# Performance work log

Measured on AMD Instinct MI355X. Metric: run time of the kernel, lower is better.

## Reference

```python
import jax, jax.numpy as jnp
import numpy as np

N, M, D = 8192, 8192, 256

def setup_inputs() -> dict:
    key = jax.random.key(0)
    kx, ky = jax.random.split(key)
    x = jax.random.normal(kx, (N, D), dtype=jnp.float32)
    y = jax.random.normal(ky, (M, D), dtype=jnp.float32)
    gamma = jnp.float32(1.0)  # learnable scalar parameter
    return {"x": x, "y": y, "gamma": gamma}

def reference(x, y, gamma):
    # Flatten trailing dims (matches x.view(x.size(0), -1))
    x = x.reshape(x.shape[0], -1)
    y = y.reshape(y.shape[0], -1)
    x_sq = jnp.sum(x * x, axis=-1)  # [N]
    y_sq = jnp.sum(y * y, axis=-1)  # [M]
    xy = x @ y.T                    # [N, M]
    sqdist = jnp.maximum(x_sq[:, None] + y_sq[None, :] - 2.0 * xy, 0.0)
    return jnp.exp(-gamma * sqdist)
```

## Files before the change

### kernel.cpp

```cpp
#include <hip/hip_runtime.h>
#include <stdint.h>


typedef __attribute__((ext_vector_type(4))) float f32x4;
typedef __attribute__((ext_vector_type(8))) int   i32x8;

#define NN 8192
#define MM 8192
#define DD 256
#define BK 128

__global__ __launch_bounds__(256) void prep_kernel(
    const float* __restrict__ x, const float* __restrict__ y,
    unsigned char* __restrict__ xb, unsigned char* __restrict__ yb,
    float* __restrict__ xsq, float* __restrict__ ysq) {
  const int lane = threadIdx.x & 63;
  const int row  = blockIdx.x * 4 + (threadIdx.x >> 6);

  const float* src = x;
  unsigned char* dst = xb;
  float* sq = xsq;
  int r = row;
  if (row >= NN) { src = y; dst = yb; sq = ysq; r = row - NN; }

  const float4 v = reinterpret_cast<const float4*>(src + (size_t)r * DD)[lane];
  float s = v.x * v.x + v.y * v.y + v.z * v.z + v.w * v.w;

  int w = 0;
  w = __builtin_amdgcn_cvt_pk_fp8_f32(v.x, v.y, w, false);
  w = __builtin_amdgcn_cvt_pk_fp8_f32(v.z, v.w, w, true);
  reinterpret_cast<int*>(dst + (size_t)r * DD)[lane] = w;

  #pragma unroll
  for (int o = 32; o > 0; o >>= 1) s += __shfl_down(s, o);
  if (lane == 0) sq[r] = s;
}

__global__ __launch_bounds__(256, 2) void rbf_gemm_kernel(
    const unsigned char* __restrict__ xb, const unsigned char* __restrict__ yb,
    const float* __restrict__ xsq, const float* __restrict__ ysq,
    const float* __restrict__ gamma, float* __restrict__ out) {
  __shared__ unsigned char As[128 * BK];
  __shared__ unsigned char Bs[128 * BK];

  const int tid   = threadIdx.x;
  const int lane  = tid & 63;
  const int wave  = tid >> 6;
  const int waveM = wave >> 1;
  const int waveN = wave & 1;
  const int row0  = blockIdx.y * 128;
  const int col0  = blockIdx.x * 128;

  f32x4 acc[4][4] = {};

  const int srow = lane >> 3;
  const int spos = lane & 7;
  const int sseg = ((spos & 1) | (((spos >> 1) ^ (srow & 3)) << 1)) * 16;

  const int fm = lane & 15;
  const int g  = lane >> 4;
  const int foff = fm * 128 + ((g ^ (fm & 3)) * 32);

  #pragma unroll
  for (int kt = 0; kt < 2; ++kt) {
    const int kk = kt * BK;
    __syncthreads();
    #pragma unroll
    for (int q = 0; q < 2; ++q) {
      const int c = wave * 2 + q;
      #pragma unroll
      for (int p = 0; p < 2; ++p) {
        const unsigned char* ga =
            yb + (size_t)(col0 + c * 16 + p * 8 + srow) * DD + kk + sseg;
        __builtin_amdgcn_global_load_lds(
            (const __attribute__((address_space(1))) void*)ga,
            (__attribute__((address_space(3))) void*)(As + c * 2048 + p * 1024),
            16, 0, 0);
        const unsigned char* gb =
            xb + (size_t)(row0 + c * 16 + p * 8 + srow) * DD + kk + sseg;
        __builtin_amdgcn_global_load_lds(
            (const __attribute__((address_space(1))) void*)gb,
            (__attribute__((address_space(3))) void*)(Bs + c * 2048 + p * 1024),
            16, 0, 0);
      }
    }
    __syncthreads();

    i32x8 a[4], b[4];
    #pragma unroll
    for (int i = 0; i < 4; ++i)
      a[i] = *reinterpret_cast<const i32x8*>(As + (waveM * 4 + i) * 2048 + foff);
    #pragma unroll
    for (int j = 0; j < 4; ++j)
      b[j] = *reinterpret_cast<const i32x8*>(Bs + (waveN * 4 + j) * 2048 + foff);

    #pragma unroll
    for (int i = 0; i < 4; ++i)
      #pragma unroll
      for (int j = 0; j < 4; ++j)
        acc[i][j] = __builtin_amdgcn_mfma_scale_f32_16x16x128_f8f6f4(
            a[i], b[j], acc[i][j], 0, 0,
            0, 0x7F7F7F7F, 0, 0x7F7F7F7F);
  }

  const float gm = gamma[0];
  const int rowb = row0 + waveN * 64 + (lane & 15);
  const int colq = col0 + waveM * 64 + (lane >> 4) * 4;

  float xsv[4];
  #pragma unroll
  for (int j = 0; j < 4; ++j) xsv[j] = xsq[rowb + j * 16];
  float4 ysv[4];
  #pragma unroll
  for (int i = 0; i < 4; ++i)
    ysv[i] = *reinterpret_cast<const float4*>(ysq + colq + i * 16);

  #pragma unroll
  for (int j = 0; j < 4; ++j) {
    const size_t obase = (size_t)(rowb + j * 16) * MM;
    #pragma unroll
    for (int i = 0; i < 4; ++i) {
      float4 v;
      float s;
      s = xsv[j] + ysv[i].x - 2.0f * acc[i][j][0]; v.x = __expf(-gm * fmaxf(s, 0.0f));
      s = xsv[j] + ysv[i].y - 2.0f * acc[i][j][1]; v.y = __expf(-gm * fmaxf(s, 0.0f));
      s = xsv[j] + ysv[i].z - 2.0f * acc[i][j][2]; v.z = __expf(-gm * fmaxf(s, 0.0f));
      s = xsv[j] + ysv[i].w - 2.0f * acc[i][j][3]; v.w = __expf(-gm * fmaxf(s, 0.0f));
      *reinterpret_cast<float4*>(out + obase + colq + i * 16) = v;
    }
  }
}

extern "C" void kernel_launch(void* const* d_in, const int* in_sizes, int n_in,
                              void* d_out, int out_size, void* d_ws, size_t ws_size,
                              hipStream_t stream) {
  const float* x     = (const float*)d_in[0];
  const float* y     = (const float*)d_in[1];
  const float* gamma = (const float*)d_in[2];
  float* out = (float*)d_out;

  unsigned char* xb = (unsigned char*)d_ws;
  unsigned char* yb = xb + (size_t)NN * DD;
  float* xsq = (float*)(yb + (size_t)MM * DD);
  float* ysq = xsq + NN;

  prep_kernel<<<(NN + MM) / 4, 256, 0, stream>>>(x, y, xb, yb, xsq, ysq);

  dim3 grid(MM / 128, NN / 128);
  rbf_gemm_kernel<<<grid, 256, 0, stream>>>(xb, yb, xsq, ysq, gamma, out);
}
```

Before: 284.0 us.

## Load FP8 MFMA fragments directly from global memory, dropping LDS staging

Removes the shared-memory tiles and the global_load_lds staging with its barriers. Each wave now reads its i32x8 MFMA fragments straight from global memory (L2/L1 cached), and occupancy is raised to 3 blocks per CU. The kernel is dominated by writing the 256 MB fp32 output, so this mainly cuts sync and LDS overhead. The cost is redundant global reads of the operand tiles across the two waves that share them.

```diff
diff --git a/kernel.cpp b/kernel.cpp
--- a/kernel.cpp
+++ b/kernel.cpp
@@ -8,7 +8,6 @@
 #define NN 8192
 #define MM 8192
 #define DD 256
-#define BK 128
 
 __global__ __launch_bounds__(256) void prep_kernel(
     const float* __restrict__ x, const float* __restrict__ y,
@@ -36,13 +35,10 @@
   if (lane == 0) sq[r] = s;
 }
 
-__global__ __launch_bounds__(256, 2) void rbf_gemm_kernel(
+__global__ __launch_bounds__(256, 3) void rbf_gemm_kernel(
     const unsigned char* __restrict__ xb, const unsigned char* __restrict__ yb,
     const float* __restrict__ xsq, const float* __restrict__ ysq,
     const float* __restrict__ gamma, float* __restrict__ out) {
-  __shared__ unsigned char As[128 * BK];
-  __shared__ unsigned char Bs[128 * BK];
-
   const int tid   = threadIdx.x;
   const int lane  = tid & 63;
   const int wave  = tid >> 6;
@@ -51,48 +47,26 @@
   const int row0  = blockIdx.y * 128;
   const int col0  = blockIdx.x * 128;
 
-  f32x4 acc[4][4] = {};
-
-  const int srow = lane >> 3;
-  const int spos = lane & 7;
-  const int sseg = ((spos & 1) | (((spos >> 1) ^ (srow & 3)) << 1)) * 16;
-
   const int fm = lane & 15;
   const int g  = lane >> 4;
-  const int foff = fm * 128 + ((g ^ (fm & 3)) * 32);
+
+  const unsigned char* abase =
+      yb + (size_t)(col0 + waveM * 64 + fm) * DD + g * 32;
+  const unsigned char* bbase =
+      xb + (size_t)(row0 + waveN * 64 + fm) * DD + g * 32;
+
+  f32x4 acc[4][4] = {};
 
   #pragma unroll
   for (int kt = 0; kt < 2; ++kt) {
-    const int kk = kt * BK;
-    __syncthreads();
-    #pragma unroll
-    for (int q = 0; q < 2; ++q) {
-      const int c = wave * 2 + q;
-      #pragma unroll
-      for (int p = 0; p < 2; ++p) {
-        const unsigned char* ga =
-            yb + (size_t)(col0 + c * 16 + p * 8 + srow) * DD + kk + sseg;
-        __builtin_amdgcn_global_load_lds(
-            (const __attribute__((address_space(1))) void*)ga,
-            (__attribute__((address_space(3))) void*)(As + c * 2048 + p * 1024),
-            16, 0, 0);
-        const unsigned char* gb =
-            xb + (size_t)(row0 + c * 16 + p * 8 + srow) * DD + kk + sseg;
-        __builtin_amdgcn_global_load_lds(
-            (const __attribute__((address_space(1))) void*)gb,
-            (__attribute__((address_space(3))) void*)(Bs + c * 2048 + p * 1024),
-            16, 0, 0);
-      }
-    }
-    __syncthreads();
-
+    const int kk = kt * 128;
     i32x8 a[4], b[4];
     #pragma unroll
     for (int i = 0; i < 4; ++i)
-      a[i] = *reinterpret_cast<const i32x8*>(As + (waveM * 4 + i) * 2048 + foff);
+      a[i] = *reinterpret_cast<const i32x8*>(abase + (size_t)i * 16 * DD + kk);
     #pragma unroll
     for (int j = 0; j < 4; ++j)
-      b[j] = *reinterpret_cast<const i32x8*>(Bs + (waveN * 4 + j) * 2048 + foff);
+      b[j] = *reinterpret_cast<const i32x8*>(bbase + (size_t)j * 16 * DD + kk);
 
     #pragma unroll
     for (int i = 0; i < 4; ++i)
```

Result: slower. 323.3 us (+13.8%).

## Process two column tiles per block with double-buffered LDS and overlapped epilogue

Applied to the files above, without the earlier changes.

Each block now computes a 128x256 output region as two 128-column tiles. The x-tile is staged once for both K halves and reused across both column tiles. The y-tile loads are double-buffered so the next global-to-LDS load is issued before the current MFMA compute, and the first tile's exp epilogue and stores run while the second tile's loads are in flight. This halves x reloads and hides load latency behind compute and stores, at the cost of twice the LDS (64KB), a second accumulator set raising register pressure, and half as many blocks.

```diff
diff --git a/kernel.cpp b/kernel.cpp
--- a/kernel.cpp
+++ b/kernel.cpp
@@ -40,8 +40,8 @@
     const unsigned char* __restrict__ xb, const unsigned char* __restrict__ yb,
     const float* __restrict__ xsq, const float* __restrict__ ysq,
     const float* __restrict__ gamma, float* __restrict__ out) {
-  __shared__ unsigned char As[128 * BK];
-  __shared__ unsigned char Bs[128 * BK];
+  __shared__ unsigned char Bs[2 * 128 * BK];
+  __shared__ unsigned char As[2][128 * BK];
 
   const int tid   = threadIdx.x;
   const int lane  = tid & 63;
@@ -49,9 +49,7 @@
   const int waveM = wave >> 1;
   const int waveN = wave & 1;
   const int row0  = blockIdx.y * 128;
-  const int col0  = blockIdx.x * 128;
-
-  f32x4 acc[4][4] = {};
+  const int col0  = blockIdx.x * 256;
 
   const int srow = lane >> 3;
   const int spos = lane & 7;
@@ -61,39 +59,45 @@
   const int g  = lane >> 4;
   const int foff = fm * 128 + ((g ^ (fm & 3)) * 32);
 
-  #pragma unroll
-  for (int kt = 0; kt < 2; ++kt) {
-    const int kk = kt * BK;
-    __syncthreads();
+  auto stageA = [&](unsigned char* dstbuf, int colt, int kk) {
     #pragma unroll
     for (int q = 0; q < 2; ++q) {
       const int c = wave * 2 + q;
       #pragma unroll
       for (int p = 0; p < 2; ++p) {
         const unsigned char* ga =
-            yb + (size_t)(col0 + c * 16 + p * 8 + srow) * DD + kk + sseg;
+            yb + (size_t)(col0 + colt + c * 16 + p * 8 + srow) * DD + kk + sseg;
         __builtin_amdgcn_global_load_lds(
             (const __attribute__((address_space(1))) void*)ga,
-            (__attribute__((address_space(3))) void*)(As + c * 2048 + p * 1024),
-            16, 0, 0);
-        const unsigned char* gb =
-            xb + (size_t)(row0 + c * 16 + p * 8 + srow) * DD + kk + sseg;
-        __builtin_amdgcn_global_load_lds(
-            (const __attribute__((address_space(1))) void*)gb,
-            (__attribute__((address_space(3))) void*)(Bs + c * 2048 + p * 1024),
+            (__attribute__((address_space(3))) void*)(dstbuf + c * 2048 + p * 1024),
             16, 0, 0);
       }
     }
-    __syncthreads();
-
+  };
+  auto stageB = [&](int kt) {
+    #pragma unroll
+    for (int q = 0; q < 2; ++q) {
+      const int c = wave * 2 + q;
+      #pragma unroll
+      for (int p = 0; p < 2; ++p) {
+        const unsigned char* gb =
+            xb + (size_t)(row0 + c * 16 + p * 8 + srow) * DD + kt * BK + sseg;
+        __builtin_amdgcn_global_load_lds(
+            (const __attribute__((address_space(1))) void*)gb,
+            (__attribute__((address_space(3))) void*)(Bs + kt * 16384 + c * 2048 + p * 1024),
+            16, 0, 0);
+      }
+    }
+  };
+  auto compute = [&](f32x4 (&acc)[4][4], const unsigned char* Abase, int kt) {
     i32x8 a[4], b[4];
+    const unsigned char* Bbase = Bs + kt * 16384;
     #pragma unroll
     for (int i = 0; i < 4; ++i)
-      a[i] = *reinterpret_cast<const i32x8*>(As + (waveM * 4 + i) * 2048 + foff);
+      a[i] = *reinterpret_cast<const i32x8*>(Abase + (waveM * 4 + i) * 2048 + foff);
     #pragma unroll
     for (int j = 0; j < 4; ++j)
-      b[j] = *reinterpret_cast<const i32x8*>(Bs + (waveN * 4 + j) * 2048 + foff);
-
+      b[j] = *reinterpret_cast<const i32x8*>(Bbase + (waveN * 4 + j) * 2048 + foff);
     #pragma unroll
     for (int i = 0; i < 4; ++i)
       #pragma unroll
@@ -101,34 +105,56 @@
         acc[i][j] = __builtin_amdgcn_mfma_scale_f32_16x16x128_f8f6f4(
             a[i], b[j], acc[i][j], 0, 0,
             0, 0x7F7F7F7F, 0, 0x7F7F7F7F);
-  }
+  };
+  const float gm = gamma[0];
+  auto epilogue = [&](const f32x4 (&acc)[4][4], int col0t) {
+    const int rowb = row0 + waveN * 64 + (lane & 15);
+    const int colq = col0t + waveM * 64 + (lane >> 4) * 4;
+    float xsv[4];
+    #pragma unroll
+    for (int j = 0; j < 4; ++j) xsv[j] = xsq[rowb + j * 16];
+    float4 ysv[4];
+    #pragma unroll
+    for (int i = 0; i < 4; ++i)
+      ysv[i] = *reinterpret_cast<const float4*>(ysq + colq + i * 16);
+    #pragma unroll
+    for (int j = 0; j < 4; ++j) {
+      const size_t obase = (size_t)(rowb + j * 16) * MM;
+      #pragma unroll
+      for (int i = 0; i < 4; ++i) {
+        float4 v;
+        float s;
+        s = xsv[j] + ysv[i].x - 2.0f * acc[i][j][0]; v.x = __expf(-gm * fmaxf(s, 0.0f));
+        s = xsv[j] + ysv[i].y - 2.0f * acc[i][j][1]; v.y = __expf(-gm * fmaxf(s, 0.0f));
+        s = xsv[j] + ysv[i].z - 2.0f * acc[i][j][2]; v.z = __expf(-gm * fmaxf(s, 0.0f));
+        s = xsv[j] + ysv[i].w - 2.0f * acc[i][j][3]; v.w = __expf(-gm * fmaxf(s, 0.0f));
+        *reinterpret_cast<float4*>(out + obase + colq + i * 16) = v;
+      }
+    }
+  };
 
-  const float gm = gamma[0];
-  const int rowb = row0 + waveN * 64 + (lane & 15);
-  const int colq = col0 + waveM * 64 + (lane >> 4) * 4;
+  f32x4 acc0[4][4] = {};
+  f32x4 acc1[4][4] = {};
 
-  float xsv[4];
-  #pragma unroll
-  for (int j = 0; j < 4; ++j) xsv[j] = xsq[rowb + j * 16];
-  float4 ysv[4];
-  #pragma unroll
-  for (int i = 0; i < 4; ++i)
-    ysv[i] = *reinterpret_cast<const float4*>(ysq + colq + i * 16);
+  stageB(0); stageB(1);
+  stageA(As[0], 0, 0);
+  __syncthreads();
 
-  #pragma unroll
-  for (int j = 0; j < 4; ++j) {
-    const size_t obase = (size_t)(rowb + j * 16) * MM;
-    #pragma unroll
-    for (int i = 0; i < 4; ++i) {
-      float4 v;
-      float s;
-      s = xsv[j] + ysv[i].x - 2.0f * acc[i][j][0]; v.x = __expf(-gm * fmaxf(s, 0.0f));
-      s = xsv[j] + ysv[i].y - 2.0f * acc[i][j][1]; v.y = __expf(-gm * fmaxf(s, 0.0f));
-      s = xsv[j] + ysv[i].z - 2.0f * acc[i][j][2]; v.z = __expf(-gm * fmaxf(s, 0.0f));
-      s = xsv[j] + ysv[i].w - 2.0f * acc[i][j][3]; v.w = __expf(-gm * fmaxf(s, 0.0f));
-      *reinterpret_cast<float4*>(out + obase + colq + i * 16) = v;
-    }
-  }
+  stageA(As[1], 0, BK);
+  compute(acc0, As[0], 0);
+  __syncthreads();
+
+  stageA(As[0], 128, 0);
+  compute(acc0, As[1], 1);
+  __syncthreads();
+
+  stageA(As[1], 128, BK);
+  compute(acc1, As[0], 0);
+  epilogue(acc0, col0);
+  __syncthreads();
+
+  compute(acc1, As[1], 1);
+  epilogue(acc1, col0 + 128);
 }
 
 extern "C" void kernel_launch(void* const* d_in, const int* in_sizes, int n_in,
@@ -146,6 +172,6 @@
 
   prep_kernel<<<(NN + MM) / 4, 256, 0, stream>>>(x, y, xb, yb, xsq, ysq);
 
-  dim3 grid(MM / 128, NN / 128);
+  dim3 grid(MM / 256, NN / 128);
   rbf_gemm_kernel<<<grid, 256, 0, stream>>>(xb, yb, xsq, ysq, gamma, out);
 }
```

Measured after the change: 293.9 us. +3.5%, slower.
